# Optimization experiments

Measured on AMD Instinct MI355X. Metric: run time of the kernel, lower is better.

Reference implementation:

```python
import jax, jax.numpy as jnp
import numpy as np

B, N, L, D = 4096, 11, 12, 256
ZDIM = 32
LINE_DIM = 64
PAST_DIM = 6 * D - (2 * D + LINE_DIM)  # 960


def _pos_enc(length, d):
    # PositionalAgentEncoding.build_pos_enc
    pos = jnp.arange(length, dtype=jnp.float32)[:, None]
    div = jnp.exp(jnp.arange(0, d, 2, dtype=jnp.float32) * (-np.log(10000.0) / d))
    pe = jnp.zeros((length, d), dtype=jnp.float32)
    pe = pe.at[:, 0::2].set(jnp.sin(pos * div))
    pe = pe.at[:, 1::2].set(jnp.cos(pos * div))
    return pe


def setup_inputs() -> dict:
    key = jax.random.key(0)
    ks = jax.random.split(key, 16)
    s = 0.02
    return {
        "inputs": jax.random.normal(ks[0], (B * N, L, 4), jnp.float32),
        "past_feature": jax.random.normal(ks[1], (B * N, PAST_DIM), jnp.float32),
        "W_in": jax.random.normal(ks[2], (4, D), jnp.float32) * s,
        "b_in": jnp.zeros((D,), jnp.float32),
        "W_pos": jax.random.normal(ks[3], (2 * D, D), jnp.float32) * s,
        "b_pos": jnp.zeros((D,), jnp.float32),
        "W_fc2": jax.random.normal(ks[4], (L * D, D), jnp.float32) * s,
        "b_fc2": jnp.zeros((D,), jnp.float32),
        "W_fc3": jax.random.normal(ks[5], (D + N, D), jnp.float32) * s,
        "b_fc3": jnp.zeros((D,), jnp.float32),
        "W_msg": jax.random.normal(ks[6], (2 * D, D), jnp.float32) * s,
        "b_msg": jnp.zeros((D,), jnp.float32),
        "W_hyp": jax.random.normal(ks[7], (2 * D, D), jnp.float32) * s,
        "b_hyp": jnp.zeros((D,), jnp.float32),
        "W_line": jax.random.normal(ks[8], (D, LINE_DIM), jnp.float32) * s,
        "W_out": jax.random.normal(ks[9], (6 * D, 128), jnp.float32) * s,
        "b_out": jnp.zeros((128,), jnp.float32),
        "W_qz": jax.random.normal(ks[10], (128, 2 * ZDIM), jnp.float32) * s,
        "b_qz": jnp.zeros((2 * ZDIM,), jnp.float32),
        "batch_size": B,
        "agent_num": N,
    }


def reference(inputs, past_feature, W_in, b_in, W_pos, b_pos, W_fc2, b_fc2,
              W_fc3, b_fc3, W_msg, b_msg, W_hyp, b_hyp, W_line,
              W_out, b_out, W_qz, b_qz, batch_size, agent_num):
    BN, length, _ = inputs.shape
    d = W_in.shape[1]
    bsz, n = batch_size, agent_num
    # input_fc + positional encoding (concat=True, dropout=eval identity)
    tf = inputs @ W_in + b_in                                   # [BN, L, D]
    pe = jnp.broadcast_to(_pos_enc(length, d), (BN, length, d))
    tf = jnp.concatenate([tf, pe], axis=-1) @ W_pos + b_pos     # [BN, L, D]
    # input_fc2 over flattened time, then category concat + input_fc3
    ftraj = tf.reshape(bsz, n, length * d) @ W_fc2 + b_fc2      # [B, N, D]
    cat = jnp.broadcast_to(jnp.eye(n, dtype=ftraj.dtype), (bsz, n, n))
    ftraj = jnp.concatenate([ftraj, cat], axis=-1) @ W_fc3 + b_fc3
    # cosine correlation + per-scene adaptive threshold
    q = ftraj / jnp.linalg.norm(ftraj, axis=2, keepdims=True)
    corr = jnp.einsum('bnd,bmd->bnm', q, q)                     # [B, N, N]
    a = corr.min(axis=(1, 2))
    thr = jnp.where(a < 0.4, 0.4,
                    jnp.where((a > 0.4) & (a < 0.6), a + 0.1, a + 0.03))
    corr = jnp.where(corr < thr[:, None, None], 0.0, corr)
    # ordinary MS_HGNN surrogate: one dense message-passing round
    attn = jax.nn.softmax(jnp.einsum('bnd,bmd->bnm', ftraj, ftraj)
                          / jnp.sqrt(jnp.asarray(d, ftraj.dtype)), axis=-1)
    agg = jnp.einsum('bnm,bmd->bnd', attn, ftraj)
    ftraj_inter = jax.nn.relu(jnp.concatenate([ftraj, agg], -1) @ W_msg + b_msg)
    # hyper/clique surrogate: binarized thresholded corr as incidence, degree-normalized
    A = (corr > 0).astype(ftraj.dtype)
    A = A / jnp.maximum(A.sum(-1, keepdims=True), 1.0)
    hag = jnp.einsum('bnm,bmd->bnd', A, ftraj)
    hyp = jax.nn.relu(jnp.concatenate([ftraj, hag], -1) @ W_hyp + b_hyp)
    feat_bs = hyp @ W_line                                      # [B, N, 64]
    final = jnp.concatenate([ftraj, ftraj_inter, feat_bs], -1).reshape(bsz * n, -1)
    h = jnp.concatenate([past_feature, final], axis=-1)         # [BN, 6D]
    h = jax.nn.relu(h @ W_out + b_out)
    return h @ W_qz + b_qz                                      # [BN, 2*zdim]
```

## Files before the change

kernel.cpp:

```cpp
#include <hip/hip_runtime.h>
#include <hip/hip_bf16.h>

#define BB 4096
#define NNA 11
#define BN (BB*NNA)

#define OFF_WEFF   0
#define OFF_BIASL  1024
#define OFF_WBIG   4096
#define OFF_WALL   16640
#define OFF_WG1F   31744
#define OFF_BIASG1 87040
#define OFF_WG2    99712
#define OFF_WQT    198656
#define OFF_P2T    202752
#define OFF_P3T    205824
#define OFF_MIX    296320
#define OFF_INTER  1287552

typedef short bh8 __attribute__((ext_vector_type(8)));
typedef float fx4 __attribute__((ext_vector_type(4)));

__device__ __forceinline__ short f2bs(float v) { __hip_bfloat16 h = __float2bfloat16(v); return *(short*)&h; }


__global__ __launch_bounds__(256) void k_p1(const float* W_in, const float* b_in,
                                            const float* W_pos, const float* b_pos,
                                            float* ws) {
  __shared__ float A[16*512];
  __shared__ float red[4*16*64];
  int t = threadIdx.x, cb = blockIdx.x;
  int ks = t >> 6, c = t & 63, col = cb*64 + c;
  float coef = -logf(10000.f) / 256.f;
  for (int i = t; i < 16*512; i += 256) {
    int row = i >> 9, kk = i & 511;
    float v;
    if (row < 4) v = (kk < 256) ? W_in[row*256 + kk] : 0.f;
    else if (kk < 256) v = b_in[kk];
    else {
      int ii = (kk - 256) >> 1;
      float dv = expf(coef * (float)(2*ii));
      float ang = (float)(row - 4) * dv;
      v = (kk & 1) ? cosf(ang) : sinf(ang);
    }
    A[i] = v;
  }
  __syncthreads();
  float acc[16];
  #pragma unroll
  for (int r = 0; r < 16; ++r) acc[r] = 0.f;
  #pragma unroll 4
  for (int j = 0; j < 128; ++j) {
    int jj = ks*128 + j;
    float b = W_pos[(size_t)jj*256 + col];
    #pragma unroll
    for (int r = 0; r < 16; ++r) acc[r] += A[r*512 + jj] * b;
  }
  #pragma unroll
  for (int r = 0; r < 16; ++r) red[(ks*16 + r)*64 + c] = acc[r];
  __syncthreads();
  for (int i = t; i < 16*64; i += 256) {
    int row = i >> 6, cc = i & 63;
    float s = red[row*64+cc] + red[(16+row)*64+cc] + red[(32+row)*64+cc] + red[(48+row)*64+cc];
    int gcol = cb*64 + cc;
    if (row < 4) ws[OFF_WEFF + row*256 + gcol] = s;
    else         ws[OFF_BIASL + (row-4)*256 + gcol] = s + b_pos[gcol];
  }
}

__global__ __launch_bounds__(256) void k_p2(const float* W_fc2, float* ws) {
  __shared__ float A[5*256];
  __shared__ float red[4*5*64];
  int t = threadIdx.x, cb = blockIdx.x, l = blockIdx.y;
  int ks = t >> 6, c = t & 63, col = cb*64 + c;
  for (int i = t; i < 5*256; i += 256) {
    int row = i >> 8, kk = i & 255;
    A[i] = (row < 4) ? ws[OFF_WEFF + row*256 + kk] : ws[OFF_BIASL + l*256 + kk];
  }
  __syncthreads();
  float acc[5] = {0.f, 0.f, 0.f, 0.f, 0.f};
  #pragma unroll 4
  for (int j = 0; j < 64; ++j) {
    int jj = ks*64 + j;
    float b = W_fc2[(size_t)(l*256 + jj)*256 + col];
    #pragma unroll
    for (int r = 0; r < 5; ++r) acc[r] += A[r*256 + jj] * b;
  }
  #pragma unroll
  for (int r = 0; r < 5; ++r) red[(ks*5 + r)*64 + c] = acc[r];
  __syncthreads();
  for (int i = t; i < 5*64; i += 256) {
    int row = i / 64, cc = i % 64;
    float s = red[row*64+cc] + red[(5+row)*64+cc] + red[(10+row)*64+cc] + red[(15+row)*64+cc];
    int gcol = cb*64 + cc;
    if (row < 4) ws[OFF_WBIG + (l*4 + row)*256 + gcol] = s;
    else         ws[OFF_P2T + l*256 + gcol] = s;
  }
}

__global__ __launch_bounds__(256) void k_p3(const float* W_fc3, const float* b_fc2, float* ws) {
  __shared__ float A[7*256];
  __shared__ float red[4*7*64];
  int t = threadIdx.x, cb = blockIdx.x, rg = blockIdx.y;
  int ks = t >> 6, c = t & 63, col = cb*64 + c;
  for (int i = t; i < 7*256; i += 256) {
    int row = i >> 8, kk = i & 255, gr = rg*7 + row;
    float v;
    if (gr < 48) v = ws[OFF_WBIG + gr*256 + kk];
    else {
      v = b_fc2[kk];
      #pragma unroll
      for (int l = 0; l < 12; ++l) v += ws[OFF_P2T + l*256 + kk];
    }
    A[i] = v;
  }
  __syncthreads();
  float acc[7] = {0.f,0.f,0.f,0.f,0.f,0.f,0.f};
  #pragma unroll 4
  for (int j = 0; j < 64; ++j) {
    int jj = ks*64 + j;
    float b = W_fc3[(size_t)jj*256 + col];
    #pragma unroll
    for (int r = 0; r < 7; ++r) acc[r] += A[r*256 + jj] * b;
  }
  #pragma unroll
  for (int r = 0; r < 7; ++r) red[(ks*7 + r)*64 + c] = acc[r];
  __syncthreads();
  for (int i = t; i < 7*64; i += 256) {
    int row = i / 64, cc = i % 64, gr = rg*7 + row;
    float s = red[row*64+cc] + red[(7+row)*64+cc] + red[(14+row)*64+cc] + red[(21+row)*64+cc];
    int gcol = cb*64 + cc;
    if (gr < 48)       ws[OFF_WALL + gr*256 + gcol] = s;
    else if (gr == 48) ws[OFF_P3T + gcol] = s;
  }
}

__device__ __forceinline__ float wg1_elem(int j, int col, const float* W_msg,
                                          const float* W_hyp, const float* W_out) {
  if (col < 256)       return W_msg[j*256 + col];
  else if (col < 512)  return W_msg[(256+j)*256 + (col-256)];
  else if (col < 768)  return W_hyp[j*256 + (col-512)];
  else if (col < 1024) return W_hyp[(256+j)*256 + (col-768)];
  else                 return W_out[(960+j)*128 + (col-1024)];
}

__global__ __launch_bounds__(256) void k_p4(const float* W_msg, const float* b_msg,
                                            const float* W_hyp, const float* b_hyp,
                                            const float* W_out, const float* W_fc3,
                                            const float* b_fc3, float* ws) {
  __shared__ float A[8*256];
  __shared__ float red[4*8*64];
  int t = threadIdx.x, cb = blockIdx.x, rg = blockIdx.y;
  int ks = t >> 6, c = t & 63, col = cb*64 + c;
  for (int i = t; i < 8*256; i += 256) {
    int row = i >> 8, kk = i & 255, gr = rg*8 + row;
    float v;
    if (gr < 48)      v = ws[OFF_WALL + gr*256 + kk];
    else if (gr < 59) v = ws[OFF_P3T + kk] + b_fc3[kk] + W_fc3[(size_t)(256 + gr - 48)*256 + kk];
    else              v = 0.f;
    A[i] = v;
  }
  __syncthreads();
  float acc[8];
  #pragma unroll
  for (int r = 0; r < 8; ++r) acc[r] = 0.f;
  #pragma unroll 4
  for (int j = 0; j < 64; ++j) {
    int jj = ks*64 + j;
    float b = wg1_elem(jj, col, W_msg, W_hyp, W_out);
    #pragma unroll
    for (int r = 0; r < 8; ++r) acc[r] += A[r*256 + jj] * b;
  }
  #pragma unroll
  for (int r = 0; r < 8; ++r) red[(ks*8 + r)*64 + c] = acc[r];
  __syncthreads();
  for (int i = t; i < 8*64; i += 256) {
    int row = i >> 6, cc = i & 63, gr = rg*8 + row;
    float s = red[row*64+cc] + red[(8+row)*64+cc] + red[(16+row)*64+cc] + red[(24+row)*64+cc];
    int gcol = cb*64 + cc;
    if (gr < 48) {
      ws[OFF_WG1F + gr*1152 + gcol] = s;
    } else if (gr < 59) {
      if (gcol < 256) s += b_msg[gcol];
      else if (gcol >= 512 && gcol < 768) s += b_hyp[gcol-512];
      ws[OFF_BIASG1 + (gr-48)*1152 + gcol] = s;
    }
  }
}

__global__ __launch_bounds__(128) void k_p5(const float* W_line, const float* W_out,
                                            const float* W_qz, float* ws) {
  int t = threadIdx.x;
  if (blockIdx.x >= 1536) {
    int i = (blockIdx.x - 1536)*128 + t;
    int n = i >> 7, k = i & 127;
    short* WQs = (short*)(ws + OFF_WQT);
    WQs[n*128 + k] = f2bs(W_qz[k*64 + n]);
    return;
  }
  int c = t, r = blockIdx.x;
  float v;
  if (r < 960)       v = W_out[r*128 + c];
  else if (r < 1216) v = W_out[(r+256)*128 + c];
  else if (r < 1472) {
    int dd = r - 1216;
    float s = 0.f;
    for (int j = 0; j < 64; ++j)
      s += W_line[dd*64 + j] * W_out[(1472+j)*128 + c];
    v = s;
  } else if (r < 1520) {
    v = ws[OFF_WG1F + (r-1472)*1152 + 1024 + c];
  } else v = 0.f;
  short* WTs = (short*)(ws + OFF_WG2);
  WTs[(size_t)c*1536 + r] = f2bs(v);
}

__global__ __launch_bounds__(256) void k_front(const float* inputs, const float* W_fc3,
                                               const float* b_fc3, float* ws) {
  __shared__ float XT[48*44];
  __shared__ float F[44*260];
  __shared__ float C[4*121];
  int t = threadIdx.x;
  int R0 = blockIdx.x * 44;
  for (int i = t; i < 44*48; i += 256) {
    int r = i / 48, k = i - r*48;
    XT[k*44 + r] = inputs[(size_t)(R0+r)*48 + k];
  }
  __syncthreads();
  {
    int d = t;
    float acc[44];
    float base = ws[OFF_P3T + d] + b_fc3[d];
    #pragma unroll
    for (int r = 0; r < 44; ++r) acc[r] = base + W_fc3[(size_t)(256 + (r % 11))*256 + d];
    for (int k = 0; k < 48; ++k) {
      float w = ws[OFF_WALL + k*256 + d];
      #pragma unroll
      for (int j = 0; j < 11; ++j) {
        float4 xv = *(const float4*)&XT[k*44 + 4*j];
        acc[4*j+0] += xv.x*w; acc[4*j+1] += xv.y*w;
        acc[4*j+2] += xv.z*w; acc[4*j+3] += xv.w*w;
      }
    }
    #pragma unroll
    for (int r = 0; r < 44; ++r) F[r*260 + d] = acc[r];
  }
  __syncthreads();
  int w = t >> 6, lane = t & 63;
  {
    const float4* F4 = (const float4*)F;
    for (int p = lane; p < 66; p += 64) {
      int n = 0, pp = p;
      while (pp >= 11 - n) { pp -= 11 - n; ++n; }
      int m = n + pp;
      int ra = (w*11 + n) * 65, rb2 = (w*11 + m) * 65;
      float s = 0.f;
      #pragma unroll 4
      for (int j = 0; j < 64; ++j) {
        float4 a = F4[ra + j], b = F4[rb2 + j];
        s += a.x*b.x + a.y*b.y + a.z*b.z + a.w*b.w;
      }
      C[w*121 + n*11 + m] = s;
      C[w*121 + m*11 + n] = s;
    }
  }
  __syncthreads();
  {
    float* Cw = C + w*121;
    float rn[11];
    #pragma unroll
    for (int n = 0; n < 11; ++n) rn[n] = 1.f / sqrtf(Cw[n*11+n]);
    float a = 1e30f;
    for (int n = 0; n < 11; ++n)
      for (int m = 0; m < 11; ++m)
        a = fminf(a, Cw[n*11+m] * rn[n] * rn[m]);
    float thr = (a < 0.4f) ? 0.4f : (((a > 0.4f) && (a < 0.6f)) ? a + 0.1f : a + 0.03f);
    int scene = blockIdx.x*4 + w;
    float* mixb = ws + OFF_MIX + (size_t)scene*242;
    if (lane < 11) {
      int n = lane;
      float mx = -1e30f;
      #pragma unroll
      for (int m = 0; m < 11; ++m) mx = fmaxf(mx, Cw[n*11+m]);
      mx *= (1.f/16.f);
      float e[11], ssum = 0.f;
      #pragma unroll
      for (int m = 0; m < 11; ++m) { e[m] = expf(Cw[n*11+m]*(1.f/16.f) - mx); ssum += e[m]; }
      float inv = 1.f / ssum;
      #pragma unroll
      for (int m = 0; m < 11; ++m) mixb[n*11+m] = e[m]*inv;
      float keep[11], cnt = 0.f;
      #pragma unroll
      for (int m = 0; m < 11; ++m) {
        float q = Cw[n*11+m] * rn[n] * rn[m];
        keep[m] = (q >= thr) ? 1.f : 0.f; cnt += keep[m];
      }
      float sc = 1.f / fmaxf(cnt, 1.f);
      #pragma unroll
      for (int m = 0; m < 11; ++m) mixb[121 + n*11 + m] = keep[m]*sc;
    }
  }
}

__global__ __launch_bounds__(256, 2) void k_mix(const float* inputs, float* ws,
                                             __hip_bfloat16* outI, __hip_bfloat16* outH) {
  __shared__ float XT[48*24];
  __shared__ float MW[4*121];
  int t = threadIdx.x;
  int s0 = blockIdx.x * 2;
  int R0 = s0 * 11;
  for (int i = t; i < 22*48; i += 256) {
    int r = i / 48, k = i - r*48;
    XT[k*24 + r] = inputs[(size_t)(R0+r)*48 + k];
  }
  for (int i = t; i < 96; i += 256) { int k = i >> 1, r = 22 + (i & 1); XT[k*24+r] = 0.f; }
  for (int i = t; i < 484; i += 256) {
    int gy = i / 242, j = i - gy*242;
    int s = j / 121, jj = j - s*121;
    MW[(gy*2 + s)*121 + jj] = ws[OFF_MIX + (size_t)(s0+s)*242 + gy*121 + jj];
  }
  __syncthreads();
  float aT0[24], aB0[24], aT1[24], aB1[24];
  #pragma unroll
  for (int r = 0; r < 24; ++r) {
    if (r < 22) {
      int nb = OFF_BIASG1 + (r % 11)*1152 + t;
      aT0[r] = ws[nb];
      aB0[r] = ws[nb + 256];
      aT1[r] = ws[nb + 512];
      aB1[r] = ws[nb + 768];
    } else { aT0[r]=0.f; aB0[r]=0.f; aT1[r]=0.f; aB1[r]=0.f; }
  }
  for (int k = 0; k < 48; ++k) {
    float wt0 = ws[OFF_WG1F + k*1152 + t];
    float wb0 = ws[OFF_WG1F + k*1152 + t + 256];
    float wt1 = ws[OFF_WG1F + k*1152 + t + 512];
    float wb1 = ws[OFF_WG1F + k*1152 + t + 768];
    #pragma unroll
    for (int j = 0; j < 6; ++j) {
      float4 xv = *(const float4*)&XT[k*24 + 4*j];
      aT0[4*j+0] += xv.x*wt0; aT0[4*j+1] += xv.y*wt0; aT0[4*j+2] += xv.z*wt0; aT0[4*j+3] += xv.w*wt0;
      aB0[4*j+0] += xv.x*wb0; aB0[4*j+1] += xv.y*wb0; aB0[4*j+2] += xv.z*wb0; aB0[4*j+3] += xv.w*wb0;
      aT1[4*j+0] += xv.x*wt1; aT1[4*j+1] += xv.y*wt1; aT1[4*j+2] += xv.z*wt1; aT1[4*j+3] += xv.w*wt1;
      aB1[4*j+0] += xv.x*wb1; aB1[4*j+1] += xv.y*wb1; aB1[4*j+2] += xv.z*wb1; aB1[4*j+3] += xv.w*wb1;
    }
  }
  #pragma unroll
  for (int s = 0; s < 2; ++s)
    #pragma unroll
    for (int n = 0; n < 11; ++n) {
      float v0 = aT0[s*11+n];
      float v1 = aT1[s*11+n];
      #pragma unroll
      for (int m = 0; m < 11; ++m) {
        v0 += MW[s*121 + n*11 + m]       * aB0[s*11+m];
        v1 += MW[(2+s)*121 + n*11 + m]   * aB1[s*11+m];
      }
      outI[(size_t)(R0 + s*11 + n)*256 + t] = __float2bfloat16(fmaxf(v0, 0.f));
      outH[(size_t)(R0 + s*11 + n)*256 + t] = __float2bfloat16(fmaxf(v1, 0.f));
    }
}

#define A_OFF 0
#define BT_OFF 4608
#define HS_OFF 0
#define WQ_OFF 8704
__global__ __launch_bounds__(256) void k_g2(const float* past, const float* inputs,
                                            const float* b_out, const float* b_qz,
                                            const __hip_bfloat16* interI, const __hip_bfloat16* hypI,
                                            float* ws, float* out) {
  __shared__ short LDS[18432];
  int t = threadIdx.x;
  int R0 = blockIdx.x * 64;
  int w = t >> 6, lane = t & 63, quad = lane >> 4, l16 = lane & 15;
  const short* WTs = (const short*)(ws + OFF_WG2);
  const short* WQs = (const short*)(ws + OFF_WQT);
  const short* intS = (const short*)interI;
  const short* hypS = (const short*)hypI;

  fx4 acc[4][2];
  #pragma unroll
  for (int mt = 0; mt < 4; ++mt)
    #pragma unroll
    for (int reg = 0; reg < 4; ++reg) {
      int nidx = (R0 + mt*16 + quad*4 + reg) % 11;
      #pragma unroll
      for (int nt = 0; nt < 2; ++nt) {
        int col = w*32 + nt*16 + l16;
        acc[mt][nt][reg] = b_out[col] + ws[OFF_BIASG1 + nidx*1152 + 1024 + col];
      }
    }

  int ar = t >> 2, akq = (t & 3) * 16;
  int bn = t >> 1, bkh = (t & 1) * 32;
  for (int ch = 0; ch < 24; ++ch) {
    __syncthreads();
    {
      short tmp[16];
      if (ch < 15) {
        const float4* sp = (const float4*)(past + (size_t)(R0+ar)*960 + ch*64 + akq);
        #pragma unroll
        for (int q = 0; q < 4; ++q) {
          float4 v = sp[q];
          tmp[4*q+0]=f2bs(v.x); tmp[4*q+1]=f2bs(v.y); tmp[4*q+2]=f2bs(v.z); tmp[4*q+3]=f2bs(v.w);
        }
        *(bh8*)&LDS[A_OFF + ar*72 + akq]     = *(bh8*)&tmp[0];
        *(bh8*)&LDS[A_OFF + ar*72 + akq + 8] = *(bh8*)&tmp[8];
      } else if (ch < 23) {
        const short* s = ((ch < 19) ? intS : hypS) + (size_t)(R0+ar)*256 + ((ch < 19) ? (ch-15) : (ch-19))*64 + akq;
        *(bh8*)&LDS[A_OFF + ar*72 + akq]     = *(const bh8*)&s[0];
        *(bh8*)&LDS[A_OFF + ar*72 + akq + 8] = *(const bh8*)&s[8];
      } else {
        if (akq < 48) {
          const float4* sp = (const float4*)(inputs + (size_t)(R0+ar)*48 + akq);
          #pragma unroll
          for (int q = 0; q < 4; ++q) {
            float4 v = sp[q];
            tmp[4*q+0]=f2bs(v.x); tmp[4*q+1]=f2bs(v.y); tmp[4*q+2]=f2bs(v.z); tmp[4*q+3]=f2bs(v.w);
          }
        } else {
          #pragma unroll
          for (int q = 0; q < 16; ++q) tmp[q] = 0;
        }
        *(bh8*)&LDS[A_OFF + ar*72 + akq]     = *(bh8*)&tmp[0];
        *(bh8*)&LDS[A_OFF + ar*72 + akq + 8] = *(bh8*)&tmp[8];
      }
    }
    {
      const short* s = WTs + (size_t)bn*1536 + ch*64 + bkh;
      #pragma unroll
      for (int q = 0; q < 4; ++q)
        *(bh8*)&LDS[BT_OFF + bn*72 + bkh + q*8] = *(const bh8*)&s[q*8];
    }
    __syncthreads();
    #pragma unroll
    for (int ks = 0; ks < 2; ++ks) {
      int kk = ks*32 + quad*8;
      bh8 a[4], b[2];
      #pragma unroll
      for (int mt = 0; mt < 4; ++mt) a[mt] = *(const bh8*)&LDS[A_OFF + (mt*16 + l16)*72 + kk];
      #pragma unroll
      for (int nt = 0; nt < 2; ++nt) b[nt] = *(const bh8*)&LDS[BT_OFF + (w*32 + nt*16 + l16)*72 + kk];
      #pragma unroll
      for (int mt = 0; mt < 4; ++mt)
        #pragma unroll
        for (int nt = 0; nt < 2; ++nt)
          acc[mt][nt] = __builtin_amdgcn_mfma_f32_16x16x32_bf16(a[mt], b[nt], acc[mt][nt], 0, 0, 0);
    }
  }
  __syncthreads();
  #pragma unroll
  for (int mt = 0; mt < 4; ++mt)
    #pragma unroll
    for (int nt = 0; nt < 2; ++nt)
      #pragma unroll
      for (int reg = 0; reg < 4; ++reg)
        LDS[HS_OFF + (mt*16 + quad*4 + reg)*136 + w*32 + nt*16 + l16] = f2bs(fmaxf(acc[mt][nt][reg], 0.f));
  {
    int n = t >> 2, kh = (t & 3) * 32;
    const short* s = WQs + n*128 + kh;
    #pragma unroll
    for (int q = 0; q < 4; ++q)
      *(bh8*)&LDS[WQ_OFF + n*136 + kh + q*8] = *(const bh8*)&s[q*8];
  }
  __syncthreads();
  fx4 acc2[4];
  {
    float bq = b_qz[w*16 + l16];
    #pragma unroll
    for (int mt = 0; mt < 4; ++mt) { acc2[mt][0]=bq; acc2[mt][1]=bq; acc2[mt][2]=bq; acc2[mt][3]=bq; }
  }
  #pragma unroll
  for (int ks = 0; ks < 4; ++ks) {
    int kk = ks*32 + quad*8;
    bh8 bb = *(const bh8*)&LDS[WQ_OFF + (w*16 + l16)*136 + kk];
    #pragma unroll
    for (int mt = 0; mt < 4; ++mt) {
      bh8 aa = *(const bh8*)&LDS[HS_OFF + (mt*16 + l16)*136 + kk];
      acc2[mt] = __builtin_amdgcn_mfma_f32_16x16x32_bf16(aa, bb, acc2[mt], 0, 0, 0);
    }
  }
  #pragma unroll
  for (int mt = 0; mt < 4; ++mt)
    #pragma unroll
    for (int reg = 0; reg < 4; ++reg)
      out[(size_t)(R0 + mt*16 + quad*4 + reg)*64 + w*16 + l16] = acc2[mt][reg];
}

extern "C" void kernel_launch(void* const* d_in, const int* in_sizes, int n_in,
                              void* d_out, int out_size, void* d_ws, size_t ws_size,
                              hipStream_t stream) {
  const float* inputs = (const float*)d_in[0];
  const float* past   = (const float*)d_in[1];
  const float* W_in   = (const float*)d_in[2];
  const float* b_in   = (const float*)d_in[3];
  const float* W_pos  = (const float*)d_in[4];
  const float* b_pos  = (const float*)d_in[5];
  const float* W_fc2  = (const float*)d_in[6];
  const float* b_fc2  = (const float*)d_in[7];
  const float* W_fc3  = (const float*)d_in[8];
  const float* b_fc3  = (const float*)d_in[9];
  const float* W_msg  = (const float*)d_in[10];
  const float* b_msg  = (const float*)d_in[11];
  const float* W_hyp  = (const float*)d_in[12];
  const float* b_hyp  = (const float*)d_in[13];
  const float* W_line = (const float*)d_in[14];
  const float* W_out  = (const float*)d_in[15];
  const float* b_out  = (const float*)d_in[16];
  const float* W_qz   = (const float*)d_in[17];
  const float* b_qz   = (const float*)d_in[18];
  float* ws = (float*)d_ws;
  __hip_bfloat16* interI = (__hip_bfloat16*)(ws + OFF_INTER);
  __hip_bfloat16* hypI   = interI + (size_t)BN*256;
  float* outp   = (float*)d_out;

  hipLaunchKernelGGL(k_p1,  dim3(4),      dim3(256), 0, stream, W_in, b_in, W_pos, b_pos, ws);
  hipLaunchKernelGGL(k_p2,  dim3(4, 12),  dim3(256), 0, stream, W_fc2, ws);
  hipLaunchKernelGGL(k_p3,  dim3(4, 7),   dim3(256), 0, stream, W_fc3, b_fc2, ws);
  hipLaunchKernelGGL(k_p4,  dim3(18, 8),  dim3(256), 0, stream, W_msg, b_msg, W_hyp, b_hyp, W_out, W_fc3, b_fc3, ws);
  hipLaunchKernelGGL(k_p5,  dim3(1600),   dim3(128), 0, stream, W_line, W_out, W_qz, ws);
  hipLaunchKernelGGL(k_front, dim3(1024), dim3(256), 0, stream, inputs, W_fc3, b_fc3, ws);
  hipLaunchKernelGGL(k_mix, dim3(2048),   dim3(256), 0, stream, inputs, ws, interI, hypI);
  hipLaunchKernelGGL(k_g2,  dim3(704),    dim3(256), 0, stream, past, inputs, b_out, b_qz,
                     interI, hypI, ws, outp);
}
```

Measured before the change: 496.0 us.

## Fuse front and mix kernels, halve k_g2 row tile for more blocks

Merges k_front and k_mix into one kernel that handles two scenes per block. The softmax and hyper mixing weights now stay in shared memory instead of going through a global workspace buffer, which also drops one kernel launch and the duplicate load of the inputs. Separately, k_g2 now processes 32 rows per block instead of 64, doubling the grid to 1408 blocks and shrinking LDS use. That gives better occupancy and SM coverage, but each block reuses the loaded weight tiles over fewer rows.

Result: no change. 503.4 us (+1.5%).

```diff
diff --git a/kernel.cpp b/kernel.cpp
--- a/kernel.cpp
+++ b/kernel.cpp
@@ -15,7 +15,6 @@
 #define OFF_WQT    198656
 #define OFF_P2T    202752
 #define OFF_P3T    205824
-#define OFF_MIX    296320
 #define OFF_INTER  1287552
 
 typedef short bh8 __attribute__((ext_vector_type(8)));
@@ -215,39 +214,43 @@
   WTs[(size_t)c*1536 + r] = f2bs(v);
 }
 
-__global__ __launch_bounds__(256) void k_front(const float* inputs, const float* W_fc3,
-                                               const float* b_fc3, float* ws) {
-  __shared__ float XT[48*44];
-  __shared__ float F[44*260];
-  __shared__ float C[4*121];
+__global__ __launch_bounds__(256, 2) void k_fm(const float* inputs, const float* W_fc3,
+                                               const float* b_fc3, float* ws,
+                                               __hip_bfloat16* outI, __hip_bfloat16* outH) {
+  __shared__ float XT[48*24];
+  __shared__ float F[22*260];
+  __shared__ float C[2*121];
+  __shared__ float MW[4*121];
   int t = threadIdx.x;
-  int R0 = blockIdx.x * 44;
-  for (int i = t; i < 44*48; i += 256) {
+  int R0 = blockIdx.x * 22;
+  for (int i = t; i < 22*48; i += 256) {
     int r = i / 48, k = i - r*48;
-    XT[k*44 + r] = inputs[(size_t)(R0+r)*48 + k];
-  }
+    XT[k*24 + r] = inputs[(size_t)(R0+r)*48 + k];
+  }
+  for (int i = t; i < 96; i += 256) { int k = i >> 1, r = 22 + (i & 1); XT[k*24+r] = 0.f; }
   __syncthreads();
   {
     int d = t;
-    float acc[44];
+    float acc[24];
     float base = ws[OFF_P3T + d] + b_fc3[d];
     #pragma unroll
-    for (int r = 0; r < 44; ++r) acc[r] = base + W_fc3[(size_t)(256 + (r % 11))*256 + d];
+    for (int r = 0; r < 24; ++r)
+      acc[r] = (r < 22) ? (base + W_fc3[(size_t)(256 + (r % 11))*256 + d]) : 0.f;
     for (int k = 0; k < 48; ++k) {
       float w = ws[OFF_WALL + k*256 + d];
       #pragma unroll
-      for (int j = 0; j < 11; ++j) {
-        float4 xv = *(const float4*)&XT[k*44 + 4*j];
+      for (int j = 0; j < 6; ++j) {
+        float4 xv = *(const float4*)&XT[k*24 + 4*j];
         acc[4*j+0] += xv.x*w; acc[4*j+1] += xv.y*w;
         acc[4*j+2] += xv.z*w; acc[4*j+3] += xv.w*w;
       }
     }
     #pragma unroll
-    for (int r = 0; r < 44; ++r) F[r*260 + d] = acc[r];
+    for (int r = 0; r < 22; ++r) F[r*260 + d] = acc[r];
   }
   __syncthreads();
   int w = t >> 6, lane = t & 63;
-  {
+  if (w < 2) {
     const float4* F4 = (const float4*)F;
     for (int p = lane; p < 66; p += 64) {
       int n = 0, pp = p;
@@ -265,7 +268,7 @@
     }
   }
   __syncthreads();
-  {
+  if (w < 2) {
     float* Cw = C + w*121;
     float rn[11];
     #pragma unroll
@@ -275,8 +278,6 @@
       for (int m = 0; m < 11; ++m)
         a = fminf(a, Cw[n*11+m] * rn[n] * rn[m]);
     float thr = (a < 0.4f) ? 0.4f : (((a > 0.4f) && (a < 0.6f)) ? a + 0.1f : a + 0.03f);
-    int scene = blockIdx.x*4 + w;
-    float* mixb = ws + OFF_MIX + (size_t)scene*242;
     if (lane < 11) {
       int n = lane;
       float mx = -1e30f;
@@ -288,7 +289,7 @@
       for (int m = 0; m < 11; ++m) { e[m] = expf(Cw[n*11+m]*(1.f/16.f) - mx); ssum += e[m]; }
       float inv = 1.f / ssum;
       #pragma unroll
-      for (int m = 0; m < 11; ++m) mixb[n*11+m] = e[m]*inv;
+      for (int m = 0; m < 11; ++m) MW[w*121 + n*11 + m] = e[m]*inv;
       float keep[11], cnt = 0.f;
       #pragma unroll
       for (int m = 0; m < 11; ++m) {
@@ -297,27 +298,8 @@
       }
       float sc = 1.f / fmaxf(cnt, 1.f);
       #pragma unroll
-      for (int m = 0; m < 11; ++m) mixb[121 + n*11 + m] = keep[m]*sc;
-    }
-  }
-}
-
-__global__ __launch_bounds__(256, 2) void k_mix(const float* inputs, float* ws,
-                                             __hip_bfloat16* outI, __hip_bfloat16* outH) {
-  __shared__ float XT[48*24];
-  __shared__ float MW[4*121];
-  int t = threadIdx.x;
-  int s0 = blockIdx.x * 2;
-  int R0 = s0 * 11;
-  for (int i = t; i < 22*48; i += 256) {
-    int r = i / 48, k = i - r*48;
-    XT[k*24 + r] = inputs[(size_t)(R0+r)*48 + k];
-  }
-  for (int i = t; i < 96; i += 256) { int k = i >> 1, r = 22 + (i & 1); XT[k*24+r] = 0.f; }
-  for (int i = t; i < 484; i += 256) {
-    int gy = i / 242, j = i - gy*242;
-    int s = j / 121, jj = j - s*121;
-    MW[(gy*2 + s)*121 + jj] = ws[OFF_MIX + (size_t)(s0+s)*242 + gy*121 + jj];
+      for (int m = 0; m < 11; ++m) MW[(2+w)*121 + n*11 + m] = keep[m]*sc;
+    }
   }
   __syncthreads();
   float aT0[24], aB0[24], aT1[24], aB1[24];
@@ -362,25 +344,25 @@
 }
 
 #define A_OFF 0
-#define BT_OFF 4608
+#define BT_OFF 2304
 #define HS_OFF 0
-#define WQ_OFF 8704
+#define WQ_OFF 4352
 __global__ __launch_bounds__(256) void k_g2(const float* past, const float* inputs,
                                             const float* b_out, const float* b_qz,
                                             const __hip_bfloat16* interI, const __hip_bfloat16* hypI,
                                             float* ws, float* out) {
-  __shared__ short LDS[18432];
+  __shared__ short LDS[13056];
   int t = threadIdx.x;
-  int R0 = blockIdx.x * 64;
+  int R0 = blockIdx.x * 32;
   int w = t >> 6, lane = t & 63, quad = lane >> 4, l16 = lane & 15;
   const short* WTs = (const short*)(ws + OFF_WG2);
   const short* WQs = (const short*)(ws + OFF_WQT);
   const short* intS = (const short*)interI;
   const short* hypS = (const short*)hypI;
 
-  fx4 acc[4][2];
-  #pragma unroll
-  for (int mt = 0; mt < 4; ++mt)
+  fx4 acc[2][2];
+  #pragma unroll
+  for (int mt = 0; mt < 2; ++mt)
     #pragma unroll
     for (int reg = 0; reg < 4; ++reg) {
       int nidx = (R0 + mt*16 + quad*4 + reg) % 11;
@@ -391,39 +373,36 @@
       }
     }
 
-  int ar = t >> 2, akq = (t & 3) * 16;
+  int ar = t >> 3, ak = (t & 7) * 8;
   int bn = t >> 1, bkh = (t & 1) * 32;
   for (int ch = 0; ch < 24; ++ch) {
     __syncthreads();
     {
-      short tmp[16];
+      short tmp[8];
       if (ch < 15) {
-        const float4* sp = (const float4*)(past + (size_t)(R0+ar)*960 + ch*64 + akq);
+        const float4* sp = (const float4*)(past + (size_t)(R0+ar)*960 + ch*64 + ak);
         #pragma unroll
-        for (int q = 0; q < 4; ++q) {
+        for (int q = 0; q < 2; ++q) {
           float4 v = sp[q];
           tmp[4*q+0]=f2bs(v.x); tmp[4*q+1]=f2bs(v.y); tmp[4*q+2]=f2bs(v.z); tmp[4*q+3]=f2bs(v.w);
         }
-        *(bh8*)&LDS[A_OFF + ar*72 + akq]     = *(bh8*)&tmp[0];
-        *(bh8*)&LDS[A_OFF + ar*72 + akq + 8] = *(bh8*)&tmp[8];
+        *(bh8*)&LDS[A_OFF + ar*72 + ak] = *(bh8*)&tmp[0];
       } else if (ch < 23) {
-        const short* s = ((ch < 19) ? intS : hypS) + (size_t)(R0+ar)*256 + ((ch < 19) ? (ch-15) : (ch-19))*64 + akq;
-        *(bh8*)&LDS[A_OFF + ar*72 + akq]     = *(const bh8*)&s[0];
-        *(bh8*)&LDS[A_OFF + ar*72 + akq + 8] = *(const bh8*)&s[8];
+        const short* s = ((ch < 19) ? intS : hypS) + (size_t)(R0+ar)*256 + ((ch < 19) ? (ch-15) : (ch-19))*64 + ak;
+        *(bh8*)&LDS[A_OFF + ar*72 + ak] = *(const bh8*)&s[0];
       } else {
-        if (akq < 48) {
-          const float4* sp = (const float4*)(inputs + (size_t)(R0+ar)*48 + akq);
+        if (ak < 48) {
+          const float4* sp = (const float4*)(inputs + (size_t)(R0+ar)*48 + ak);
           #pragma unroll
-          for (int q = 0; q < 4; ++q) {
+          for (int q = 0; q < 2; ++q) {
             float4 v = sp[q];
             tmp[4*q+0]=f2bs(v.x); tmp[4*q+1]=f2bs(v.y); tmp[4*q+2]=f2bs(v.z); tmp[4*q+3]=f2bs(v.w);
           }
         } else {
           #pragma unroll
-          for (int q = 0; q < 16; ++q) tmp[q] = 0;
+          for (int q = 0; q < 8; ++q) tmp[q] = 0;
         }
-        *(bh8*)&LDS[A_OFF + ar*72 + akq]     = *(bh8*)&tmp[0];
-        *(bh8*)&LDS[A_OFF + ar*72 + akq + 8] = *(bh8*)&tmp[8];
+        *(bh8*)&LDS[A_OFF + ar*72 + ak] = *(bh8*)&tmp[0];
       }
     }
     {
@@ -436,13 +415,13 @@
     #pragma unroll
     for (int ks = 0; ks < 2; ++ks) {
       int kk = ks*32 + quad*8;
-      bh8 a[4], b[2];
-      #pragma unroll
-      for (int mt = 0; mt < 4; ++mt) a[mt] = *(const bh8*)&LDS[A_OFF + (mt*16 + l16)*72 + kk];
+      bh8 a[2], b[2];
+      #pragma unroll
+      for (int mt = 0; mt < 2; ++mt) a[mt] = *(const bh8*)&LDS[A_OFF + (mt*16 + l16)*72 + kk];
       #pragma unroll
       for (int nt = 0; nt < 2; ++nt) b[nt] = *(const bh8*)&LDS[BT_OFF + (w*32 + nt*16 + l16)*72 + kk];
       #pragma unroll
-      for (int mt = 0; mt < 4; ++mt)
+      for (int mt = 0; mt < 2; ++mt)
         #pragma unroll
         for (int nt = 0; nt < 2; ++nt)
           acc[mt][nt] = __builtin_amdgcn_mfma_f32_16x16x32_bf16(a[mt], b[nt], acc[mt][nt], 0, 0, 0);
@@ -450,7 +429,7 @@
   }
   __syncthreads();
   #pragma unroll
-  for (int mt = 0; mt < 4; ++mt)
+  for (int mt = 0; mt < 2; ++mt)
     #pragma unroll
     for (int nt = 0; nt < 2; ++nt)
       #pragma unroll
@@ -464,24 +443,24 @@
       *(bh8*)&LDS[WQ_OFF + n*136 + kh + q*8] = *(const bh8*)&s[q*8];
   }
   __syncthreads();
-  fx4 acc2[4];
+  fx4 acc2[2];
   {
     float bq = b_qz[w*16 + l16];
     #pragma unroll
-    for (int mt = 0; mt < 4; ++mt) { acc2[mt][0]=bq; acc2[mt][1]=bq; acc2[mt][2]=bq; acc2[mt][3]=bq; }
+    for (int mt = 0; mt < 2; ++mt) { acc2[mt][0]=bq; acc2[mt][1]=bq; acc2[mt][2]=bq; acc2[mt][3]=bq; }
   }
   #pragma unroll
   for (int ks = 0; ks < 4; ++ks) {
     int kk = ks*32 + quad*8;
     bh8 bb = *(const bh8*)&LDS[WQ_OFF + (w*16 + l16)*136 + kk];
     #pragma unroll
-    for (int mt = 0; mt < 4; ++mt) {
+    for (int mt = 0; mt < 2; ++mt) {
       bh8 aa = *(const bh8*)&LDS[HS_OFF + (mt*16 + l16)*136 + kk];
       acc2[mt] = __builtin_amdgcn_mfma_f32_16x16x32_bf16(aa, bb, acc2[mt], 0, 0, 0);
     }
   }
   #pragma unroll
-  for (int mt = 0; mt < 4; ++mt)
+  for (int mt = 0; mt < 2; ++mt)
     #pragma unroll
     for (int reg = 0; reg < 4; ++reg)
       out[(size_t)(R0 + mt*16 + quad*4 + reg)*64 + w*16 + l16] = acc2[mt][reg];
@@ -519,8 +498,7 @@
   hipLaunchKernelGGL(k_p3,  dim3(4, 7),   dim3(256), 0, stream, W_fc3, b_fc2, ws);
   hipLaunchKernelGGL(k_p4,  dim3(18, 8),  dim3(256), 0, stream, W_msg, b_msg, W_hyp, b_hyp, W_out, W_fc3, b_fc3, ws);
   hipLaunchKernelGGL(k_p5,  dim3(1600),   dim3(128), 0, stream, W_line, W_out, W_qz, ws);
-  hipLaunchKernelGGL(k_front, dim3(1024), dim3(256), 0, stream, inputs, W_fc3, b_fc3, ws);
-  hipLaunchKernelGGL(k_mix, dim3(2048),   dim3(256), 0, stream, inputs, ws, interI, hypI);
-  hipLaunchKernelGGL(k_g2,  dim3(704),    dim3(256), 0, stream, past, inputs, b_out, b_qz,
+  hipLaunchKernelGGL(k_fm,  dim3(2048),   dim3(256), 0, stream, inputs, W_fc3, b_fc3, ws, interI, hypI);
+  hipLaunchKernelGGL(k_g2,  dim3(1408),   dim3(256), 0, stream, past, inputs, b_out, b_qz,
                      interI, hypI, ws, outp);
 }
```
